# Performance work log

Hardware: AMD Instinct MI355X
Metric: run time of the kernel (lower is better)

Reference implementation:

```python
import jax, jax.numpy as jnp
import numpy as np
from jax import lax

T, D, HID, C = 16384, 1024, 1024, 16
H = HID // 2  # per-direction hidden size


def _uniform(key, shape, bound):
    return jax.random.uniform(key, shape, jnp.float32, -bound, bound)


def setup_inputs() -> dict:
    key = jax.random.key(0)
    ks = jax.random.split(key, 16)
    s = 1.0 / np.sqrt(H)        # PyTorch LSTM init bound
    sl = 1.0 / np.sqrt(HID)     # PyTorch Linear init bound
    return {
        "sequence": jax.random.normal(ks[0], (T, D), jnp.float32),
        "h0": jax.random.normal(ks[1], (2, 1, H), jnp.float32),
        "c0": jax.random.normal(ks[2], (2, 1, H), jnp.float32),
        "w_ih_f": _uniform(ks[3], (4 * H, D), s),
        "w_hh_f": _uniform(ks[4], (4 * H, H), s),
        "b_ih_f": _uniform(ks[5], (4 * H,), s),
        "b_hh_f": _uniform(ks[6], (4 * H,), s),
        "w_ih_b": _uniform(ks[7], (4 * H, D), s),
        "w_hh_b": _uniform(ks[8], (4 * H, H), s),
        "b_ih_b": _uniform(ks[9], (4 * H,), s),
        "b_hh_b": _uniform(ks[10], (4 * H,), s),
        "w_lin": _uniform(ks[11], (C, HID), sl),
        "b_lin": _uniform(ks[12], (C,), sl),
        "transitions": jax.random.uniform(ks[13], (C, C), jnp.float32),  # torch.rand
    }


def _lstm_scan(x, h0, c0, w_ih, w_hh, b_ih, b_hh, reverse):
    # x: [T, D]; PyTorch gate order: i, f, g, o
    def step(carry, xt):
        h, c = carry
        g = w_ih @ xt + b_ih + w_hh @ h + b_hh  # [4H]
        i, f, gg, o = jnp.split(g, 4)
        i = jax.nn.sigmoid(i)
        f = jax.nn.sigmoid(f)
        gg = jnp.tanh(gg)
        o = jax.nn.sigmoid(o)
        c = f * c + i * gg
        h = o * jnp.tanh(c)
        return (h, c), h
    _, hs = lax.scan(step, (h0, c0), x, reverse=reverse)
    return hs  # [T, H], hs[t] = hidden at time t (aligned for both directions)


def _viterbi(feats, transitions):
    # feats: [T, C]; init forward_var = zeros (per the original torch.full(..., 0))
    def vstep(fv, feat):
        scores = fv[None, :] + transitions          # [C_next, C_prev]
        bp = jnp.argmax(scores, axis=1)             # backpointers
        fv2 = jnp.max(scores, axis=1) + feat
        return fv2, bp
    fv, bps = lax.scan(vstep, jnp.zeros((C,), feats.dtype), feats)
    best = jnp.argmax(fv)
    path_score = fv[best]
    def bstep(b, bp_row):
        nb = bp_row[b]
        return nb, nb
    _, rev = lax.scan(bstep, best, bps, reverse=True)  # rev[t] = state before step t's transition
    best_path = jnp.concatenate([rev, best[None]])     # length T+1, matches torch output
    return path_score, best_path


def reference(sequence, h0, c0, w_ih_f, w_hh_f, b_ih_f, b_hh_f,
              w_ih_b, w_hh_b, b_ih_b, b_hh_b, w_lin, b_lin, transitions):
    hs_f = _lstm_scan(sequence, h0[0, 0], c0[0, 0], w_ih_f, w_hh_f, b_ih_f, b_hh_f, False)
    hs_b = _lstm_scan(sequence, h0[1, 0], c0[1, 0], w_ih_b, w_hh_b, b_ih_b, b_hh_b, True)
    lstm_out = jnp.concatenate([hs_f, hs_b], axis=-1)   # [T, HID]
    feats = lstm_out @ w_lin.T + b_lin                  # [T, C]
    return _viterbi(feats, transitions)
```

## Files before the change

### kernel.cpp

```cpp
#include <hip/hip_runtime.h>

#define T_STEPS 16384
#define CSTEPS  1024
#define NCHUNK  16
#define DMODEL  1024
#define HID     512
#define G4      2048
#define NC      16
#define NGEMMB  192

static const size_t OFF_Z     = 0;
static const size_t OFF_HF    = 8388608ull;
static const size_t OFF_HB    = 16777216ull;
static const size_t OFF_FEATS = 25165824ull;
static const size_t FLOATS_TOTAL = 25427968ull;
static const size_t OFF_BP_B  = FLOATS_TOTAL * 4ull;
static const size_t OFF_P_B   = OFF_BP_B + 262144ull;
static const size_t OFF_EX_B  = OFF_P_B + 262144ull;
static const size_t OFF_CTR_B = OFF_EX_B + 16384ull;
static const size_t NEED_B    = OFF_CTR_B + 256ull;

__global__ __launch_bounds__(256, 1) void fused_kernel(
    const float* __restrict__ seq,
    const float* __restrict__ wih_f, const float* __restrict__ bih_f, const float* __restrict__ bhh_f,
    const float* __restrict__ wih_b, const float* __restrict__ bih_b, const float* __restrict__ bhh_b,
    const float* __restrict__ whh_f, const float* __restrict__ whh_b,
    const float* __restrict__ h0, const float* __restrict__ c0,
    float* __restrict__ hf, float* __restrict__ hb,
    float* __restrict__ Zbuf,
    unsigned long long* __restrict__ exf, unsigned long long* __restrict__ exb,
    unsigned int* __restrict__ gemm_done, unsigned int* __restrict__ recur_prog)
{
    const int bid = blockIdx.x;
    const int tid = threadIdx.x;

    if (bid < 64) {
        const int dir = bid >> 5;
        const int g   = bid & 31;
        const float* whh = dir ? whh_b : whh_f;
        float* hout      = dir ? hb : hf;
        unsigned long long* ex = dir ? exb : exf;

        const int w = tid >> 6, lane = tid & 63;
        const int G = lane >> 4, u = lane & 15;
        const int R = 512 * G + 16 * g + u;

        float wreg[128];
        {
            const float* src = &whh[(size_t)R * HID + w * 128];
            #pragma unroll
            for (int j = 0; j < 32; ++j) {
                float4 v = *(const float4*)&src[j * 4];
                wreg[j*4+0]=v.x; wreg[j*4+1]=v.y; wreg[j*4+2]=v.z; wreg[j*4+3]=v.w;
            }
        }

        __shared__ __align__(16) float h_lds[512];
        __shared__ __align__(16) float p_lds[2][256];

        float cst = 0.f;
        if (w == 0 && lane < 16) cst = c0[dir * HID + 16 * g + lane];

        {
            const int i0 = 128 * w + 2 * lane;
            h_lds[i0]     = h0[dir * HID + i0];
            h_lds[i0 + 1] = h0[dir * HID + i0 + 1];
        }

        int dead = 0;
        const float* Zd = Zbuf + (size_t)dir * 2 * CSTEPS * G4;

        for (int s = 0; s < T_STEPS; ++s) {
            if ((s & (CSTEPS - 1)) == 0) {
                if (tid == 0) {
                    const int cg = s >> 10;
                    int guard = 0; unsigned int gd;
                    do {
                        gd = __hip_atomic_load(&gemm_done[cg], __ATOMIC_RELAXED,
                                               __HIP_MEMORY_SCOPE_AGENT);
                        if (++guard > (1 << 20)) { dead = 1; break; }
                    } while (gd < (unsigned)NGEMMB);
                }
                if (__syncthreads_or(dead)) break;
            }
            const int c   = s >> 10;
            const int par = s & 1;
            const int t   = dir ? (T_STEPS - 1 - s) : s;
            const int rr  = dir ? (1023 - (s & 1023)) : (s & 1023);

            float zr = 0.f;
            if (w == 0)
                zr = __hip_atomic_load(&Zd[((size_t)(c & 1) * CSTEPS + rr) * G4 + R],
                                       __ATOMIC_RELAXED, __HIP_MEMORY_SCOPE_AGENT);

            if (s > 0) {
                const unsigned long long want = (unsigned long long)(unsigned)s;
                const int i0 = 128 * w + 2 * lane;
                unsigned long long v0, v1;
                int guard = 0;
                for (;;) {
                    v0 = __hip_atomic_load(&ex[par*512 + i0],     __ATOMIC_RELAXED, __HIP_MEMORY_SCOPE_AGENT);
                    v1 = __hip_atomic_load(&ex[par*512 + i0 + 1], __ATOMIC_RELAXED, __HIP_MEMORY_SCOPE_AGENT);
                    if (((v0 >> 32) == want) & ((v1 >> 32) == want)) break;
                    if (++guard > (1 << 16)) { dead = 1; break; }
                }
                union { unsigned int ui; float f; } ca, cb;
                ca.ui = (unsigned int)v0; cb.ui = (unsigned int)v1;
                h_lds[i0]     = ca.f;
                h_lds[i0 + 1] = cb.f;
            }

            float acc = 0.f;
            {
                const float4* h4 = (const float4*)&h_lds[w * 128];
                #pragma unroll
                for (int j = 0; j < 32; ++j) {
                    float4 hv = h4[j];
                    acc += wreg[j*4+0]*hv.x + wreg[j*4+1]*hv.y
                         + wreg[j*4+2]*hv.z + wreg[j*4+3]*hv.w;
                }
            }
            p_lds[par][tid] = acc;
            if (__syncthreads_or(dead)) break;

            if (w == 0) {
                float rv = p_lds[par][lane] + p_lds[par][64+lane]
                         + p_lds[par][128+lane] + p_lds[par][192+lane] + zr;
                float a = (G == 2) ? tanhf(rv) : 1.f / (1.f + expf(-rv));
                float ig = __shfl(a, u,      64);
                float fg = __shfl(a, u + 16, 64);
                float gg = __shfl(a, u + 32, 64);
                float og = __shfl(a, u + 48, 64);
                if (lane < 16) {
                    float cn = fg * cst + ig * gg;
                    cst = cn;
                    float hn = og * tanhf(cn);
                    union { float f; unsigned int ui; } cv; cv.f = hn;
                    __hip_atomic_store(&ex[((s + 1) & 1) * 512 + 16 * g + lane],
                        ((unsigned long long)(unsigned)(s + 1) << 32) | (unsigned long long)cv.ui,
                        __ATOMIC_RELAXED, __HIP_MEMORY_SCOPE_AGENT);
                    hout[(size_t)t * HID + 16 * g + lane] = hn;
                }
                if ((s & (CSTEPS - 1)) == (CSTEPS - 1) && lane == 0)
                    __hip_atomic_fetch_add(&recur_prog[c], 1u, __ATOMIC_RELAXED,
                                           __HIP_MEMORY_SCOPE_AGENT);
            }
        }
    } else {
        const int gb = bid - 64;
        __shared__ __align__(16) float As[16][68];
        __shared__ __align__(16) float Bs[16][68];
        const int lr = tid >> 2, ls = tid & 3, tx = tid & 15, ty = tid >> 4;

        for (int cc = 0; cc < NCHUNK; ++cc) {
            if (cc >= 2 && tid == 0) {
                int guard = 0; unsigned int rp;
                do {
                    rp = __hip_atomic_load(&recur_prog[cc - 2], __ATOMIC_RELAXED,
                                           __HIP_MEMORY_SCOPE_AGENT);
                    if (++guard > (1 << 20)) break;
                } while (rp < 64u);
            }
            __syncthreads();

            for (int tix = gb; tix < 2 * 16 * 32; tix += NGEMMB) {
                const int dr  = tix >> 9;
                const int rem = tix & 511;
                const int mt  = rem >> 5;
                const int nt  = rem & 31;
                const int t0  = dr ? (T_STEPS - (cc + 1) * CSTEPS) : (cc * CSTEPS);
                const float* W  = dr ? wih_b : wih_f;
                const float* bi = dr ? bih_b : bih_f;
                const float* bh = dr ? bhh_b : bhh_f;
                float* Zt = Zbuf + (size_t)(dr * 2 + (cc & 1)) * CSTEPS * G4;

                float acc[4][4] = {};
                for (int k0 = 0; k0 < DMODEL; k0 += 16) {
                    float4 av = *(const float4*)&seq[(size_t)(t0 + mt*64 + lr) * DMODEL + k0 + ls*4];
                    float4 bv = *(const float4*)&W[(size_t)(nt*64 + lr) * DMODEL + k0 + ls*4];
                    __syncthreads();
                    As[ls*4+0][lr]=av.x; As[ls*4+1][lr]=av.y; As[ls*4+2][lr]=av.z; As[ls*4+3][lr]=av.w;
                    Bs[ls*4+0][lr]=bv.x; Bs[ls*4+1][lr]=bv.y; Bs[ls*4+2][lr]=bv.z; Bs[ls*4+3][lr]=bv.w;
                    __syncthreads();
                    #pragma unroll
                    for (int k = 0; k < 16; ++k) {
                        float4 a = *(const float4*)&As[k][ty * 4];
                        float4 b = *(const float4*)&Bs[k][tx * 4];
                        acc[0][0]+=a.x*b.x; acc[0][1]+=a.x*b.y; acc[0][2]+=a.x*b.z; acc[0][3]+=a.x*b.w;
                        acc[1][0]+=a.y*b.x; acc[1][1]+=a.y*b.y; acc[1][2]+=a.y*b.z; acc[1][3]+=a.y*b.w;
                        acc[2][0]+=a.z*b.x; acc[2][1]+=a.z*b.y; acc[2][2]+=a.z*b.z; acc[2][3]+=a.z*b.w;
                        acc[3][0]+=a.w*b.x; acc[3][1]+=a.w*b.y; acc[3][2]+=a.w*b.z; acc[3][3]+=a.w*b.w;
                    }
                }
                float4 b4  = *(const float4*)&bi[nt * 64 + tx * 4];
                float4 c4v = *(const float4*)&bh[nt * 64 + tx * 4];
                float bx=b4.x+c4v.x, by=b4.y+c4v.y, bz=b4.z+c4v.z, bw_=b4.w+c4v.w;
                #pragma unroll
                for (int i = 0; i < 4; ++i) {
                    float4 o;
                    o.x=acc[i][0]+bx; o.y=acc[i][1]+by; o.z=acc[i][2]+bz; o.w=acc[i][3]+bw_;
                    *(float4*)&Zt[(size_t)(mt*64 + ty*4 + i) * G4 + nt*64 + tx*4] = o;
                }
            }
            __threadfence();
            __syncthreads();
            if (tid == 0)
                __hip_atomic_fetch_add(&gemm_done[cc], 1u, __ATOMIC_RELEASE,
                                       __HIP_MEMORY_SCOPE_AGENT);
        }
    }
}

__global__ __launch_bounds__(256) void feats_kernel(
    const float* __restrict__ hf, const float* __restrict__ hb,
    const float* __restrict__ wlin, const float* __restrict__ blin,
    float* __restrict__ feats)
{
    const int t = blockIdx.x;
    __shared__ __align__(16) float hl[1024];
    const int tid = threadIdx.x;
    {
        const float* src = (tid < 128) ? &hf[(size_t)t * HID + tid * 4]
                                       : &hb[(size_t)t * HID + (tid - 128) * 4];
        *(float4*)&hl[tid * 4] = *(const float4*)src;
    }
    __syncthreads();
    const int c = tid >> 4, p = tid & 15;
    float s = 0.0f;
    #pragma unroll
    for (int j = 0; j < 16; ++j) {
        float4 h4 = *(const float4*)&hl[p * 4 + j * 64];
        float4 w4 = *(const float4*)&wlin[(size_t)c * 1024 + p * 4 + j * 64];
        s += h4.x*w4.x + h4.y*w4.y + h4.z*w4.z + h4.w*w4.w;
    }
    s += __shfl_down(s, 8, 16);
    s += __shfl_down(s, 4, 16);
    s += __shfl_down(s, 2, 16);
    s += __shfl_down(s, 1, 16);
    if (p == 0) feats[t * NC + c] = s + blin[c];
}

__global__ __launch_bounds__(64) void viterbi_kernel(
    const float* __restrict__ feats, const float* __restrict__ trans,
    unsigned char* __restrict__ bp, float* __restrict__ out,
    unsigned int* __restrict__ bT)
{
    __shared__ __align__(16) float fl[4096];
    __shared__ __align__(16) float fvs[16];
    const int l = threadIdx.x;
    float tr[16];
    if (l < 16) {
        #pragma unroll
        for (int j = 0; j < 16; ++j) tr[j] = trans[l * 16 + j];
    }
    float fv = 0.0f;
    for (int cb = 0; cb < 64; ++cb) {
        #pragma unroll
        for (int j = 0; j < 16; ++j)
            *(float4*)&fl[j * 256 + l * 4] =
                *(const float4*)&feats[cb * 4096 + j * 256 + l * 4];
        __syncthreads();
        if (l < 16) {
            for (int k = 0; k < 256; ++k) {
                float m = __shfl(fv, 0, 16) + tr[0];
                int bi = 0;
                #pragma unroll
                for (int j = 1; j < 16; ++j) {
                    float sc = __shfl(fv, j, 16) + tr[j];
                    if (sc > m) { m = sc; bi = j; }
                }
                bp[(size_t)(cb * 256 + k) * 16 + l] = (unsigned char)bi;
                fv = m + fl[k * 16 + l];
            }
        }
        __syncthreads();
    }
    if (l < 16) fvs[l] = fv;
    __syncthreads();
    if (l == 0) {
        float best = fvs[0]; int bi = 0;
        #pragma unroll
        for (int j = 1; j < 16; ++j) if (fvs[j] > best) { best = fvs[j]; bi = j; }
        out[0] = best;
        out[1 + T_STEPS] = (float)bi;
        *bT = (unsigned int)bi;
    }
}

__global__ __launch_bounds__(64) void maps_kernel(
    const unsigned char* __restrict__ bp, unsigned char* __restrict__ P)
{
    const int j = blockIdx.x;
    const int l = threadIdx.x;
    __shared__ __align__(16) unsigned char lb[4096];
    __shared__ __align__(16) unsigned char lp[4096];
    #pragma unroll
    for (int i = 0; i < 4; ++i)
        *(uint4*)&lb[i * 1024 + l * 16] = *(const uint4*)&bp[(size_t)j * 4096 + i * 1024 + l * 16];
    __syncthreads();
    if (l < 16) {
        int cur = l;
        for (int k = 255; k >= 0; --k) {
            cur = lb[k * 16 + cur];
            lp[k * 16 + l] = (unsigned char)cur;
        }
    }
    __syncthreads();
    #pragma unroll
    for (int i = 0; i < 4; ++i)
        *(uint4*)&P[(size_t)j * 4096 + i * 1024 + l * 16] = *(const uint4*)&lp[i * 1024 + l * 16];
}

__global__ __launch_bounds__(64) void path_kernel(
    const unsigned char* __restrict__ P, const unsigned int* __restrict__ bT,
    float* __restrict__ out)
{
    const int j = blockIdx.x;
    const int l = threadIdx.x;
    int e = (int)(*bT);
    for (int i = 63; i > j; --i) e = P[(size_t)i * 4096 + e];
    for (int k = l; k < 256; k += 64)
        out[1 + j * 256 + k] = (float)P[(size_t)j * 4096 + k * 16 + e];
}

__global__ void fb_kernel(float* out, int n, float v0) {
    int i = blockIdx.x * 256 + threadIdx.x;
    if (i < n) out[i] = (i == 0) ? v0 : 0.0f;
}

extern "C" void kernel_launch(void* const* d_in, const int* in_sizes, int n_in,
                              void* d_out, int out_size, void* d_ws, size_t ws_size,
                              hipStream_t stream) {
    const float* seq   = (const float*)d_in[0];
    const float* h0    = (const float*)d_in[1];
    const float* c0    = (const float*)d_in[2];
    const float* wih_f = (const float*)d_in[3];
    const float* whh_f = (const float*)d_in[4];
    const float* bih_f = (const float*)d_in[5];
    const float* bhh_f = (const float*)d_in[6];
    const float* wih_b = (const float*)d_in[7];
    const float* whh_b = (const float*)d_in[8];
    const float* bih_b = (const float*)d_in[9];
    const float* bhh_b = (const float*)d_in[10];
    const float* wlin  = (const float*)d_in[11];
    const float* blin  = (const float*)d_in[12];
    const float* trans = (const float*)d_in[13];
    float* out = (float*)d_out;

    if (ws_size < NEED_B) {
        fb_kernel<<<(out_size + 255) / 256, 256, 0, stream>>>(out, out_size, -(float)ws_size);
        return;
    }

    float* wsf = (float*)d_ws;
    float* Zbuf  = wsf + OFF_Z;
    float* hf    = wsf + OFF_HF;
    float* hb    = wsf + OFF_HB;
    float* feats = wsf + OFF_FEATS;
    unsigned char* bp = (unsigned char*)d_ws + OFF_BP_B;
    unsigned char* P  = (unsigned char*)d_ws + OFF_P_B;
    unsigned long long* exf = (unsigned long long*)((char*)d_ws + OFF_EX_B);
    unsigned long long* exb = exf + 1024;
    unsigned int* ctr = (unsigned int*)((char*)d_ws + OFF_CTR_B);
    unsigned int* gemm_done  = ctr;
    unsigned int* recur_prog = ctr + 16;
    unsigned int* bT         = ctr + 32;

    hipMemsetAsync((void*)exf, 0, 16384 + 256, stream);

    {
        void* args[] = { (void*)&seq,
                         (void*)&wih_f, (void*)&bih_f, (void*)&bhh_f,
                         (void*)&wih_b, (void*)&bih_b, (void*)&bhh_b,
                         (void*)&whh_f, (void*)&whh_b,
                         (void*)&h0, (void*)&c0,
                         (void*)&hf, (void*)&hb, (void*)&Zbuf,
                         (void*)&exf, (void*)&exb,
                         (void*)&gemm_done, (void*)&recur_prog };
        hipError_t e = hipLaunchCooperativeKernel(
            reinterpret_cast<void*>(fused_kernel), dim3(256), dim3(256),
            args, 0, stream);
        if (e != hipSuccess) {
            fused_kernel<<<256, 256, 0, stream>>>(
                seq, wih_f, bih_f, bhh_f, wih_b, bih_b, bhh_b,
                whh_f, whh_b, h0, c0, hf, hb, Zbuf, exf, exb,
                gemm_done, recur_prog);
        }
    }

    feats_kernel<<<16384, 256, 0, stream>>>(hf, hb, wlin, blin, feats);
    viterbi_kernel<<<1, 64, 0, stream>>>(feats, trans, bp, out, bT);
    maps_kernel<<<64, 64, 0, stream>>>(bp, P);
    path_kernel<<<64, 64, 0, stream>>>(P, bT, out);
}
```

Baseline: 43.74 ms.

## Co-locate recurrent blocks on one XCD and exchange hidden state via L2-coherent loads

Recurrent blocks are remapped (bid&7) so that, under round-robin XCD dispatch, each direction's 32 blocks land on the same XCD. Blocks verify this with XCC_ID and a vote. When co-located, the per-step hidden-state exchange uses sc0 dwordx4 loads and stores that stay in the XCD-local L2 instead of device-scope atomics, with a mirrored device-scope buffer as fallback. The Z gate-input load is also prefetched one step ahead and folded into wave 1's partial sum, taking global latency off the critical path. This adds startup handshakes, duplicate stores and reliance on the hardware's dispatch mapping.

```diff
diff --git a/kernel.cpp b/kernel.cpp
--- a/kernel.cpp
+++ b/kernel.cpp
@@ -9,6 +9,9 @@
 #define NC      16
 #define NGEMMB  192
 
+#define FAST_GUARD (1 << 14)
+#define SLOW_GUARD (1 << 18)
+
 static const size_t OFF_Z     = 0;
 static const size_t OFF_HF    = 8388608ull;
 static const size_t OFF_HB    = 16777216ull;
@@ -17,8 +20,25 @@
 static const size_t OFF_BP_B  = FLOATS_TOTAL * 4ull;
 static const size_t OFF_P_B   = OFF_BP_B + 262144ull;
 static const size_t OFF_EX_B  = OFF_P_B + 262144ull;
-static const size_t OFF_CTR_B = OFF_EX_B + 16384ull;
-static const size_t NEED_B    = OFF_CTR_B + 256ull;
+static const size_t OFF_CTR_B = OFF_EX_B + 32768ull;
+static const size_t NEED_B    = OFF_CTR_B + 1024ull;
+
+typedef unsigned int u32x4 __attribute__((ext_vector_type(4)));
+
+__device__ __forceinline__ unsigned read_xcc_id() {
+    unsigned x;
+    asm volatile("s_getreg_b32 %0, hwreg(HW_REG_XCC_ID)" : "=s"(x));
+    return x & 15u;
+}
+__device__ __forceinline__ u32x4 load_x4_sc0(const unsigned long long* p) {
+    u32x4 r;
+    asm volatile("global_load_dwordx4 %0, %1, off sc0\n\ts_waitcnt vmcnt(0)"
+                 : "=&v"(r) : "v"(p) : "memory");
+    return r;
+}
+__device__ __forceinline__ void store_x2_sc0(unsigned long long* p, unsigned long long v) {
+    asm volatile("global_store_dwordx2 %0, %1, off sc0" :: "v"(p), "v"(v) : "memory");
+}
 
 __global__ __launch_bounds__(256, 1) void fused_kernel(
     const float* __restrict__ seq,
@@ -28,22 +48,30 @@
     const float* __restrict__ h0, const float* __restrict__ c0,
     float* __restrict__ hf, float* __restrict__ hb,
     float* __restrict__ Zbuf,
-    unsigned long long* __restrict__ exf, unsigned long long* __restrict__ exb,
-    unsigned int* __restrict__ gemm_done, unsigned int* __restrict__ recur_prog)
+    unsigned long long* __restrict__ exf,
+    unsigned int* __restrict__ gemm_done, unsigned int* __restrict__ recur_prog,
+    unsigned int* __restrict__ xcdid, unsigned int* __restrict__ fastvote)
 {
     const int bid = blockIdx.x;
     const int tid = threadIdx.x;
-
-    if (bid < 64) {
-        const int dir = bid >> 5;
-        const int g   = bid & 31;
+    const int pk  = bid & 7;
+
+    if (pk < 2) {
+        const int dir = pk;
+        const int g   = bid >> 3;
         const float* whh = dir ? whh_b : whh_f;
         float* hout      = dir ? hb : hf;
-        unsigned long long* ex = dir ? exb : exf;
+        unsigned long long* ex  = dir ? (exf + 1024) : exf;
+        unsigned long long* exm = ex + 2048;
 
         const int w = tid >> 6, lane = tid & 63;
         const int G = lane >> 4, u = lane & 15;
         const int R = 512 * G + 16 * g + u;
+
+        const unsigned xcc = read_xcc_id();
+        if (tid == 0)
+            __hip_atomic_store(&xcdid[dir*32+g], 0x100u | xcc,
+                               __ATOMIC_RELAXED, __HIP_MEMORY_SCOPE_AGENT);
 
         float wreg[128];
         {
@@ -55,6 +83,32 @@
             }
         }
 
+        int mism = 0;
+        if (tid < 32) {
+            unsigned v; int gu = 0;
+            do {
+                v = __hip_atomic_load(&xcdid[dir*32+tid], __ATOMIC_RELAXED,
+                                      __HIP_MEMORY_SCOPE_AGENT);
+                if (++gu > (1 << 20)) { v = 0xFFFFFFFFu; break; }
+            } while (!(v & 0x100u));
+            mism = (v == 0xFFFFFFFFu) || ((v & 15u) != xcc);
+        }
+        const int myfast = !__syncthreads_or(mism);
+        if (tid == 0)
+            __hip_atomic_store(&fastvote[dir*32+g], 0x100u | (unsigned)myfast,
+                               __ATOMIC_RELAXED, __HIP_MEMORY_SCOPE_AGENT);
+        int bad2 = 0;
+        if (tid < 32) {
+            unsigned v; int gu = 0;
+            do {
+                v = __hip_atomic_load(&fastvote[dir*32+tid], __ATOMIC_RELAXED,
+                                      __HIP_MEMORY_SCOPE_AGENT);
+                if (++gu > (1 << 20)) { v = 0x100u; break; }
+            } while (!(v & 0x100u));
+            bad2 = !(v & 1u);
+        }
+        int lfast = !__syncthreads_or(bad2);
+
         __shared__ __align__(16) float h_lds[512];
         __shared__ __align__(16) float p_lds[2][256];
 
@@ -69,8 +123,10 @@
 
         int dead = 0;
         const float* Zd = Zbuf + (size_t)dir * 2 * CSTEPS * G4;
+        float zr_cur = 0.f, zr_pref = 0.f;
 
         for (int s = 0; s < T_STEPS; ++s) {
+            const int par = s & 1;
             if ((s & (CSTEPS - 1)) == 0) {
                 if (tid == 0) {
                     const int cg = s >> 10;
@@ -82,32 +138,51 @@
                     } while (gd < (unsigned)NGEMMB);
                 }
                 if (__syncthreads_or(dead)) break;
-            }
-            const int c   = s >> 10;
-            const int par = s & 1;
-            const int t   = dir ? (T_STEPS - 1 - s) : s;
-            const int rr  = dir ? (1023 - (s & 1023)) : (s & 1023);
-
-            float zr = 0.f;
-            if (w == 0)
-                zr = __hip_atomic_load(&Zd[((size_t)(c & 1) * CSTEPS + rr) * G4 + R],
-                                       __ATOMIC_RELAXED, __HIP_MEMORY_SCOPE_AGENT);
+                if (w == 1) {
+                    const int rr = dir ? (1023 - (s & 1023)) : (s & 1023);
+                    zr_cur = __hip_atomic_load(
+                        &Zd[((size_t)((s >> 10) & 1) * CSTEPS + rr) * G4 + R],
+                        __ATOMIC_RELAXED, __HIP_MEMORY_SCOPE_AGENT);
+                }
+            } else if (w == 1) {
+                zr_cur = zr_pref;
+            }
 
             if (s > 0) {
-                const unsigned long long want = (unsigned long long)(unsigned)s;
-                const int i0 = 128 * w + 2 * lane;
-                unsigned long long v0, v1;
-                int guard = 0;
-                for (;;) {
-                    v0 = __hip_atomic_load(&ex[par*512 + i0],     __ATOMIC_RELAXED, __HIP_MEMORY_SCOPE_AGENT);
-                    v1 = __hip_atomic_load(&ex[par*512 + i0 + 1], __ATOMIC_RELAXED, __HIP_MEMORY_SCOPE_AGENT);
-                    if (((v0 >> 32) == want) & ((v1 >> 32) == want)) break;
-                    if (++guard > (1 << 16)) { dead = 1; break; }
-                }
-                union { unsigned int ui; float f; } ca, cb;
-                ca.ui = (unsigned int)v0; cb.ui = (unsigned int)v1;
-                h_lds[i0]     = ca.f;
-                h_lds[i0 + 1] = cb.f;
+                const int i0   = 128 * w + 2 * lane;
+                const int base = par * 512 + i0;
+                const unsigned want = (unsigned)s;
+                int got = 0;
+                if (lfast) {
+                    int guard = 0;
+                    for (;;) {
+                        u32x4 q = load_x4_sc0(&ex[base]);
+                        if (q.y == want && q.w == want) {
+                            union { unsigned ui; float f; } a, b;
+                            a.ui = q.x; b.ui = q.z;
+                            h_lds[i0]     = a.f;
+                            h_lds[i0 + 1] = b.f;
+                            got = 1; break;
+                        }
+                        if (++guard > FAST_GUARD) break;
+                    }
+                    if (!got) lfast = 0;
+                }
+                if (!got) {
+                    const unsigned long long wl = (unsigned long long)want;
+                    unsigned long long v0, v1;
+                    int guard = 0;
+                    for (;;) {
+                        v0 = __hip_atomic_load(&exm[base],     __ATOMIC_RELAXED, __HIP_MEMORY_SCOPE_AGENT);
+                        v1 = __hip_atomic_load(&exm[base + 1], __ATOMIC_RELAXED, __HIP_MEMORY_SCOPE_AGENT);
+                        if (((v0 >> 32) == wl) & ((v1 >> 32) == wl)) break;
+                        if (++guard > SLOW_GUARD) { dead = 1; break; }
+                    }
+                    union { unsigned int ui; float f; } ca, cb;
+                    ca.ui = (unsigned int)v0; cb.ui = (unsigned int)v1;
+                    h_lds[i0]     = ca.f;
+                    h_lds[i0 + 1] = cb.f;
+                }
             }
 
             float acc = 0.f;
@@ -120,12 +195,20 @@
                          + wreg[j*4+2]*hv.z + wreg[j*4+3]*hv.w;
                 }
             }
+            if (w == 1) acc += zr_cur;
             p_lds[par][tid] = acc;
+            if (w == 1 && ((s + 1) & (CSTEPS - 1)) != 0) {
+                const int sn = s + 1;
+                const int rr = dir ? (1023 - (sn & 1023)) : (sn & 1023);
+                zr_pref = __hip_atomic_load(
+                    &Zd[((size_t)((sn >> 10) & 1) * CSTEPS + rr) * G4 + R],
+                    __ATOMIC_RELAXED, __HIP_MEMORY_SCOPE_AGENT);
+            }
             if (__syncthreads_or(dead)) break;
 
             if (w == 0) {
                 float rv = p_lds[par][lane] + p_lds[par][64+lane]
-                         + p_lds[par][128+lane] + p_lds[par][192+lane] + zr;
+                         + p_lds[par][128+lane] + p_lds[par][192+lane];
                 float a = (G == 2) ? tanhf(rv) : 1.f / (1.f + expf(-rv));
                 float ig = __shfl(a, u,      64);
                 float fg = __shfl(a, u + 16, 64);
@@ -136,18 +219,22 @@
                     cst = cn;
                     float hn = og * tanhf(cn);
                     union { float f; unsigned int ui; } cv; cv.f = hn;
-                    __hip_atomic_store(&ex[((s + 1) & 1) * 512 + 16 * g + lane],
-                        ((unsigned long long)(unsigned)(s + 1) << 32) | (unsigned long long)cv.ui,
-                        __ATOMIC_RELAXED, __HIP_MEMORY_SCOPE_AGENT);
+                    unsigned long long pv =
+                        ((unsigned long long)(unsigned)(s + 1) << 32) | (unsigned long long)cv.ui;
+                    const int slot = ((s + 1) & 1) * 512 + 16 * g + lane;
+                    store_x2_sc0(&ex[slot], pv);
+                    __hip_atomic_store(&exm[slot], pv, __ATOMIC_RELAXED,
+                                       __HIP_MEMORY_SCOPE_AGENT);
+                    const int t = dir ? (T_STEPS - 1 - s) : s;
                     hout[(size_t)t * HID + 16 * g + lane] = hn;
                 }
                 if ((s & (CSTEPS - 1)) == (CSTEPS - 1) && lane == 0)
-                    __hip_atomic_fetch_add(&recur_prog[c], 1u, __ATOMIC_RELAXED,
+                    __hip_atomic_fetch_add(&recur_prog[s >> 10], 1u, __ATOMIC_RELAXED,
                                            __HIP_MEMORY_SCOPE_AGENT);
             }
         }
     } else {
-        const int gb = bid - 64;
+        const int gb = (pk - 2) * 32 + (bid >> 3);
         __shared__ __align__(16) float As[16][68];
         __shared__ __align__(16) float Bs[16][68];
         const int lr = tid >> 2, ls = tid & 3, tx = tid & 15, ty = tid >> 4;
@@ -360,13 +447,14 @@
     unsigned char* bp = (unsigned char*)d_ws + OFF_BP_B;
     unsigned char* P  = (unsigned char*)d_ws + OFF_P_B;
     unsigned long long* exf = (unsigned long long*)((char*)d_ws + OFF_EX_B);
-    unsigned long long* exb = exf + 1024;
     unsigned int* ctr = (unsigned int*)((char*)d_ws + OFF_CTR_B);
     unsigned int* gemm_done  = ctr;
     unsigned int* recur_prog = ctr + 16;
     unsigned int* bT         = ctr + 32;
-
-    hipMemsetAsync((void*)exf, 0, 16384 + 256, stream);
+    unsigned int* xcdid      = ctr + 64;
+    unsigned int* fastvote   = ctr + 128;
+
+    hipMemsetAsync((void*)exf, 0, 32768 + 1024, stream);
 
     {
         void* args[] = { (void*)&seq,
@@ -375,16 +463,17 @@
                          (void*)&whh_f, (void*)&whh_b,
                          (void*)&h0, (void*)&c0,
                          (void*)&hf, (void*)&hb, (void*)&Zbuf,
-                         (void*)&exf, (void*)&exb,
-                         (void*)&gemm_done, (void*)&recur_prog };
+                         (void*)&exf,
+                         (void*)&gemm_done, (void*)&recur_prog,
+                         (void*)&xcdid, (void*)&fastvote };
         hipError_t e = hipLaunchCooperativeKernel(
             reinterpret_cast<void*>(fused_kernel), dim3(256), dim3(256),
             args, 0, stream);
         if (e != hipSuccess) {
             fused_kernel<<<256, 256, 0, stream>>>(
                 seq, wih_f, bih_f, bhh_f, wih_b, bih_b, bhh_b,
-                whh_f, whh_b, h0, c0, hf, hb, Zbuf, exf, exb,
-                gemm_done, recur_prog);
+                whh_f, whh_b, h0, c0, hf, hb, Zbuf, exf,
+                gemm_done, recur_prog, xcdid, fastvote);
         }
     }
 
```

Result: slower. 65.37 ms (+49.4%).
